# Kernel tuning notes

Measured on AMD Instinct MI355X. Metric: run time of the kernel, lower is better.

The kernel has to match this reference:

```python
import jax, jax.numpy as jnp
import numpy as np
from functools import partial

B, C, COND, L_MEL, HOP, UP = 4, 32, 80, 2048, 8, 8
LAYERS, K, HID, KPK, EMB = 4, 3, 64, 3, 512
L_AUD = L_MEL * UP  # 16384


def conv1d(x, w, b=None, padding=0, dilation=1):
    # x: (B, Cin, L), w: (Cout, Cin, K) -- PyTorch Conv1d semantics
    out = jax.lax.conv_general_dilated(
        x, w, window_strides=(1,), padding=[(padding, padding)],
        rhs_dilation=(dilation,), dimension_numbers=('NCH', 'OIH', 'NCH'))
    if b is not None:
        out = out + b[None, :, None]
    return out


def conv_transpose1d(x, w, stride, pad):
    # PyTorch ConvTranspose1d, weight (Cin, Cout, K), no bias, output_padding=0
    k = w.shape[-1]
    w_eq = jnp.flip(w, -1).transpose(1, 0, 2)  # (Cout, Cin, K)
    lo = k - 1 - pad
    return jax.lax.conv_general_dilated(
        x, w_eq, window_strides=(1,), padding=[(lo, lo)],
        lhs_dilation=(stride,), dimension_numbers=('NCH', 'OIH', 'NCH'))


def lrelu(x, s):
    return jnp.where(x >= 0, x, s * x)


def kernel_predictor(cond, kp_in_w, kp_in_b, kp_res_w1, kp_res_b1,
                     kp_res_w2, kp_res_b2, kp_k_w, kp_k_b, kp_b_w, kp_b_b):
    # FastDiff/UnivNet KernelPredictor: input conv (k=5) + 3 residual blocks + heads
    h = lrelu(conv1d(cond, kp_in_w, kp_in_b, padding=2), 0.1)
    for i in range(3):  # fixed small structural loop
        r = lrelu(conv1d(h, kp_res_w1[i], kp_res_b1[i], padding=1), 0.1)
        r = lrelu(conv1d(r, kp_res_w2[i], kp_res_b2[i], padding=1), 0.1)
        h = h + r
    bsz, _, ln = cond.shape
    k = conv1d(h, kp_k_w, kp_k_b, padding=1)
    b = conv1d(h, kp_b_w, kp_b_b, padding=1)
    kernels = k.reshape(bsz, LAYERS, C, 2 * C, K, ln)
    bias = b.reshape(bsz, LAYERS, 2 * C, ln)
    return kernels, bias


def location_variable_convolution(x, kernel, bias, dilation, hop):
    # x: (B, Cin, L), kernel: (B, Cin, Cout, K, Lf), bias: (B, Cout, Lf)
    bsz, cin, ln = x.shape
    _, _, cout, ks, lf = kernel.shape
    pad = dilation * (ks - 1) // 2
    xp = jnp.pad(x, ((0, 0), (0, 0), (pad, pad)))
    # gather per-frame sliding windows: (Lf, hop, K)
    pos = (jnp.arange(lf) * hop)[:, None, None] \
        + jnp.arange(hop)[None, :, None] \
        + (jnp.arange(ks) * dilation)[None, None, :]
    xw = xp[:, :, pos]  # (B, Cin, Lf, hop, K)
    o = jnp.einsum('bilsk,biokl->bols', xw, kernel)  # (B, Cout, Lf, hop)
    o = o + bias[:, :, :, None]
    return o.reshape(bsz, cout, lf * hop)


def forward(x, audio_down, c, noise_embedding, fc_t_w, fc_t_b, up_w, conv_w,
            kp_in_w, kp_in_b, kp_res_w1, kp_res_b1, kp_res_w2, kp_res_b2,
            kp_k_w, kp_k_b, kp_b_w, kp_b_b):
    noise = (noise_embedding @ fc_t_w.T + fc_t_b)[:, :, None]  # (B, 80, 1)
    condition = c + noise
    kernels, bias = kernel_predictor(condition, kp_in_w, kp_in_b, kp_res_w1,
                                     kp_res_b1, kp_res_w2, kp_res_b2,
                                     kp_k_w, kp_k_b, kp_b_w, kp_b_b)
    h = lrelu(x, 0.2)
    h = conv_transpose1d(h, up_w, UP, UP // 2)  # (B, 32, 16384)
    for i in range(LAYERS):
        h = h + audio_down
        y = lrelu(h, 0.2)
        y = conv1d(y, conv_w[i], padding=3 ** i, dilation=3 ** i)
        y = lrelu(y, 0.2)
        y = location_variable_convolution(y, kernels[:, i], bias[:, i], 1, HOP)
        h = h + jax.nn.sigmoid(y[:, :C, :]) * jnp.tanh(y[:, C:, :])
    return h


def setup_inputs() -> dict:
    key = jax.random.key(0)
    ks = jax.random.split(key, 20)
    s = 0.02
    kch = LAYERS * C * (2 * C) * K  # 24576
    bch = LAYERS * 2 * C            # 256
    return {
        'x': jax.random.normal(ks[0], (B, C, L_MEL), jnp.float32),
        'audio_down': jax.random.normal(ks[1], (B, C, L_AUD), jnp.float32),
        'c': jax.random.normal(ks[2], (B, COND, L_MEL), jnp.float32),
        'noise_embedding': jax.random.normal(ks[3], (B, EMB), jnp.float32),
        'fc_t_w': jax.random.normal(ks[4], (COND, EMB), jnp.float32) * s,
        'fc_t_b': jnp.zeros((COND,), jnp.float32),
        'up_w': jax.random.normal(ks[5], (C, C, UP * 2), jnp.float32) * s,
        'conv_w': jax.random.normal(ks[6], (LAYERS, C, C, K), jnp.float32) * s,
        'kp_in_w': jax.random.normal(ks[7], (HID, COND, 5), jnp.float32) * s,
        'kp_in_b': jnp.zeros((HID,), jnp.float32),
        'kp_res_w1': jax.random.normal(ks[8], (3, HID, HID, KPK), jnp.float32) * s,
        'kp_res_b1': jnp.zeros((3, HID), jnp.float32),
        'kp_res_w2': jax.random.normal(ks[9], (3, HID, HID, KPK), jnp.float32) * s,
        'kp_res_b2': jnp.zeros((3, HID), jnp.float32),
        'kp_k_w': jax.random.normal(ks[10], (kch, HID, KPK), jnp.float32) * s,
        'kp_k_b': jnp.zeros((kch,), jnp.float32),
        'kp_b_w': jax.random.normal(ks[11], (bch, HID, KPK), jnp.float32) * s,
        'kp_b_b': jnp.zeros((bch,), jnp.float32),
    }


def reference(x, audio_down, c, noise_embedding, fc_t_w, fc_t_b, up_w, conv_w,
              kp_in_w, kp_in_b, kp_res_w1, kp_res_b1, kp_res_w2, kp_res_b2,
              kp_k_w, kp_k_b, kp_b_w, kp_b_b):
    return forward(x, audio_down, c, noise_embedding, fc_t_w, fc_t_b, up_w,
                   conv_w, kp_in_w, kp_in_b, kp_res_w1, kp_res_b1, kp_res_w2,
                   kp_res_b2, kp_k_w, kp_k_b, kp_b_w, kp_b_b)
```

## Files before the change

kernel.cpp:

```cpp
#include <hip/hip_runtime.h>
#include <math.h>

#define B_      4
#define C_      32
#define COND_   80
#define LMEL_   2048
#define HOP_    8
#define UP_     8
#define LAYERS_ 4
#define K_      3
#define HID_    64
#define KPK_    3
#define EMB_    512
#define LAUD_   (LMEL_*UP_)
#define KCH_    (LAYERS_*C_*2*C_*K_)
#define BCH_    (LAYERS_*2*C_)

typedef short v8s __attribute__((ext_vector_type(8)));
typedef float v4f __attribute__((ext_vector_type(4)));

__device__ __forceinline__ float lrelu_(float v, float s) { return v >= 0.f ? v : s * v; }

__device__ __forceinline__ unsigned short f2bf(float f) {
  unsigned int x = __float_as_uint(f);
  unsigned int r = (x + 0x7FFFu + ((x >> 16) & 1u)) >> 16;
  return (unsigned short)r;
}

__global__ void k_noise_cond(const float* __restrict__ ne, const float* __restrict__ fw,
                             const float* __restrict__ fb, const float* __restrict__ c,
                             float* __restrict__ cond) {
  int b = blockIdx.x / COND_;
  int cc = blockIdx.x % COND_;
  __shared__ float red[256];
  float p = 0.f;
  for (int j = threadIdx.x; j < EMB_; j += 256)
    p += ne[b*EMB_ + j] * fw[cc*EMB_ + j];
  red[threadIdx.x] = p;
  __syncthreads();
  for (int s = 128; s > 0; s >>= 1) {
    if (threadIdx.x < s) red[threadIdx.x] += red[threadIdx.x + s];
    __syncthreads();
  }
  float noise = red[0] + fb[cc];
  const float* cp = c + (b*COND_ + cc)*LMEL_;
  float* op = cond + (b*COND_ + cc)*LMEL_;
  for (int l = threadIdx.x; l < LMEL_; l += 256) op[l] = cp[l] + noise;
}

__global__ __launch_bounds__(256) void k_kp_in(const float* __restrict__ cond, const float* __restrict__ w,
                                               const float* __restrict__ bias, float* __restrict__ out) {
  const int T = 32;
  int b  = blockIdx.x / (LMEL_/T);
  int lb = (blockIdx.x % (LMEL_/T)) * T;
  __shared__ float sc[COND_][T + 4];
  for (int idx = threadIdx.x; idx < COND_*(T+4); idx += 256) {
    int cc = idx / (T+4), j = idx % (T+4);
    int l = lb + j - 2;
    sc[cc][j] = (l >= 0 && l < LMEL_) ? cond[(b*COND_ + cc)*LMEL_ + l] : 0.f;
  }
  __syncthreads();
  int ch = threadIdx.x & 63;
  int lq = threadIdx.x >> 6;
  float acc[8];
#pragma unroll
  for (int ii = 0; ii < 8; ii++) acc[ii] = bias[ch];
  const float* wr = w + ch*COND_*5;
  for (int cc = 0; cc < COND_; cc++) {
    float r[12];
#pragma unroll
    for (int j = 0; j < 12; j++) r[j] = sc[cc][lq*8 + j];
#pragma unroll
    for (int k = 0; k < 5; k++) {
      float wv = wr[cc*5 + k];
#pragma unroll
      for (int ii = 0; ii < 8; ii++) acc[ii] = fmaf(wv, r[ii + k], acc[ii]);
    }
  }
  float* op = out + (b*HID_ + ch)*LMEL_ + lb + lq*8;
#pragma unroll
  for (int ii = 0; ii < 8; ii++) acc[ii] = lrelu_(acc[ii], 0.1f);
  *reinterpret_cast<float4*>(&op[0]) = make_float4(acc[0], acc[1], acc[2], acc[3]);
  *reinterpret_cast<float4*>(&op[4]) = make_float4(acc[4], acc[5], acc[6], acc[7]);
}

__global__ __launch_bounds__(256) void k_kp_res(const float* __restrict__ in, const float* __restrict__ w,
                                                const float* __restrict__ bias, const float* __restrict__ res,
                                                float* __restrict__ out) {
  const int T = 32;
  int b  = blockIdx.x / (LMEL_/T);
  int lb = (blockIdx.x % (LMEL_/T)) * T;
  __shared__ float si[HID_][T + 4];
  for (int idx = threadIdx.x; idx < HID_*(T+2); idx += 256) {
    int cc = idx / (T+2), j = idx % (T+2);
    int l = lb + j - 1;
    si[cc][j] = (l >= 0 && l < LMEL_) ? in[(b*HID_ + cc)*LMEL_ + l] : 0.f;
  }
  __syncthreads();
  int ch = threadIdx.x & 63;
  int lq = threadIdx.x >> 6;
  float acc[8];
#pragma unroll
  for (int ii = 0; ii < 8; ii++) acc[ii] = bias[ch];
  const float* wr = w + ch*HID_*3;
  for (int cc = 0; cc < HID_; cc++) {
    float r[10];
#pragma unroll
    for (int j = 0; j < 10; j++) r[j] = si[cc][lq*8 + j];
#pragma unroll
    for (int k = 0; k < 3; k++) {
      float wv = wr[cc*3 + k];
#pragma unroll
      for (int ii = 0; ii < 8; ii++) acc[ii] = fmaf(wv, r[ii + k], acc[ii]);
    }
  }
  int lo = lb + lq*8;
  float* op = out + (b*HID_ + ch)*LMEL_ + lo;
  const float* rp = res ? res + (b*HID_ + ch)*LMEL_ + lo : nullptr;
#pragma unroll
  for (int ii = 0; ii < 8; ii++) {
    acc[ii] = lrelu_(acc[ii], 0.1f);
    if (rp) acc[ii] += rp[ii];
  }
  *reinterpret_cast<float4*>(&op[0]) = make_float4(acc[0], acc[1], acc[2], acc[3]);
  *reinterpret_cast<float4*>(&op[4]) = make_float4(acc[4], acc[5], acc[6], acc[7]);
}

__global__ __launch_bounds__(256) void k_kp_bias(const float* __restrict__ in, const float* __restrict__ w,
                                                 const float* __restrict__ bias, float* __restrict__ out) {
  const int T = 16;
  int b  = blockIdx.x / (LMEL_/T);
  int lb = (blockIdx.x % (LMEL_/T)) * T;
  __shared__ float si[HID_][T + 2];
  for (int idx = threadIdx.x; idx < HID_*(T+2); idx += 256) {
    int cc = idx / (T+2), j = idx % (T+2);
    int l = lb + j - 1;
    si[cc][j] = (l >= 0 && l < LMEL_) ? in[(b*HID_ + cc)*LMEL_ + l] : 0.f;
  }
  __syncthreads();
  int ch = threadIdx.x;
  float acc[T];
  float bv = bias[ch];
#pragma unroll
  for (int ii = 0; ii < T; ii++) acc[ii] = bv;
  const float* wr = w + ch*HID_*3;
  for (int cc = 0; cc < HID_; cc++) {
    float w0 = wr[cc*3], w1 = wr[cc*3+1], w2 = wr[cc*3+2];
#pragma unroll
    for (int ii = 0; ii < T; ii++)
      acc[ii] = fmaf(w0, si[cc][ii], fmaf(w1, si[cc][ii+1], fmaf(w2, si[cc][ii+2], acc[ii])));
  }
  float* op = out + (b*BCH_ + ch)*LMEL_ + lb;
#pragma unroll
  for (int q = 0; q < 4; q++)
    *reinterpret_cast<float4*>(&op[q*4]) = make_float4(acc[q*4], acc[q*4+1], acc[q*4+2], acc[q*4+3]);
}

__global__ void k_mkUp(const float* __restrict__ upw, float* __restrict__ wt) {
  int idx = blockIdx.x*256 + threadIdx.x;
  if (idx >= C_*C_*16) return;
  int co = idx & 31, j = (idx >> 5) & 15, ci = idx >> 9;
  wt[idx] = upw[(ci*C_ + co)*16 + j];
}

#define UT 32
__global__ __launch_bounds__(256) void k_upsample(const float* __restrict__ x, const float* __restrict__ wt,
                                                  float* __restrict__ h) {
  int b  = blockIdx.x / 65;
  int s0 = (blockIdx.x % 65) * UT;
  __shared__ float sw[16384];
  __shared__ float sx[C_][33 + 3];
  for (int idx = threadIdx.x*4; idx < 16384; idx += 1024)
    *reinterpret_cast<float4*>(&sw[idx]) = *reinterpret_cast<const float4*>(&wt[idx]);
  for (int idx = threadIdx.x; idx < C_*33; idx += 256) {
    int ci = idx / 33, i = idx % 33;
    int s = s0 - 1 + i;
    float v = (s >= 0 && s < LMEL_) ? x[(b*C_ + ci)*LMEL_ + s] : 0.f;
    sx[ci][i] = lrelu_(v, 0.2f);
  }
  __syncthreads();
  int co = threadIdx.x & 31, sq = threadIdx.x >> 5;
  float acc[4][8];
#pragma unroll
  for (int k = 0; k < 4; k++)
#pragma unroll
    for (int r = 0; r < 8; r++) acc[k][r] = 0.f;
  for (int ci = 0; ci < C_; ci++) {
    float xv[5];
#pragma unroll
    for (int m = 0; m < 5; m++) xv[m] = sx[ci][sq*4 + m];
    const float* wl = &sw[ci*512 + co];
#pragma unroll
    for (int r = 0; r < 8; r++) {
      float wa = wl[r*32];
      float wb = wl[(r+8)*32];
#pragma unroll
      for (int k = 0; k < 4; k++)
        acc[k][r] = fmaf(wa, xv[k+1], fmaf(wb, xv[k], acc[k][r]));
    }
  }
  float* op = h + ((size_t)b*C_ + co)*LAUD_;
#pragma unroll
  for (int k = 0; k < 4; k++) {
    int s1 = s0 + sq*4 + k;
    int lo = 8*s1 - 4;
    if (lo >= 0 && lo + 4 <= LAUD_)
      *reinterpret_cast<float4*>(&op[lo]) = make_float4(acc[k][0], acc[k][1], acc[k][2], acc[k][3]);
    if (lo >= -4 && lo + 8 <= LAUD_)
      *reinterpret_cast<float4*>(&op[lo+4]) = make_float4(acc[k][4], acc[k][5], acc[k][6], acc[k][7]);
  }
}

__global__ void k_mkA(const float* __restrict__ kw, unsigned short* __restrict__ waf) {
  int idx = blockIdx.x*256 + threadIdx.x;
  if (idx >= KCH_*HID_*KPK_) return;
  int i    = idx & 7;
  int lane = (idx >> 3) & 63;
  int ks   = (idx >> 9) % 6;
  int tile = (idx / 3072) & 3;
  int rk   = idx / 12288;
  int layer = rk / 96, rem = rk % 96, ci = rem / 3, kk = rem % 3;
  int cout = tile*16 + (lane & 15);
  int j    = ks*32 + ((lane >> 4) << 3) + i;
  int row  = ((layer*32 + ci)*64 + cout)*3 + kk;
  waf[idx] = f2bf(kw[row*192 + j]);
}

__global__ void k_mkKbT(const float* __restrict__ kb, float* __restrict__ kbt) {
  int idx = blockIdx.x*256 + threadIdx.x;
  if (idx >= KCH_) return;
  int cr = idx & 15, tile = (idx >> 4) & 3, rk = idx >> 6;
  int layer = rk / 96, rem = rk % 96, ci = rem / 3, kk = rem % 3;
  int cout = tile*16 + cr;
  kbt[idx] = kb[((layer*32 + ci)*64 + cout)*3 + kk];
}

template<int DIL>
__global__ __launch_bounds__(256) void k_dilconv(const float* __restrict__ h, const float* __restrict__ ad,
                                                 const float* __restrict__ w, float* __restrict__ y2) {
  const int T = 128;
  int b  = blockIdx.x / (LAUD_/T);
  int tb = (blockIdx.x % (LAUD_/T)) * T;
  const int W = T + 2*DIL;
  __shared__ float ss[C_][T + 2*27 + 4];
  for (int idx = threadIdx.x; idx < C_*W; idx += 256) {
    int ci = idx / W, j = idx % W;
    int t = tb - DIL + j;
    float v = 0.f;
    if (t >= 0 && t < LAUD_) {
      int g = (b*C_ + ci)*LAUD_ + t;
      v = h[g] + ad[g];
    }
    ss[ci][j] = lrelu_(v, 0.2f);
  }
  __syncthreads();
  int co = threadIdx.x & 31, tq = threadIdx.x >> 5;
  float acc[16];
#pragma unroll
  for (int ii = 0; ii < 16; ii++) acc[ii] = 0.f;
  const float* wr = w + co*C_*3;
  for (int ci = 0; ci < C_; ci++) {
    float w0 = wr[ci*3], w1 = wr[ci*3+1], w2 = wr[ci*3+2];
#pragma unroll
    for (int ii = 0; ii < 16; ii++) {
      int tl = tq*16 + ii;
      acc[ii] = fmaf(w0, ss[ci][tl], fmaf(w1, ss[ci][tl + DIL], fmaf(w2, ss[ci][tl + 2*DIL], acc[ii])));
    }
  }
  float* op = y2 + (b*C_ + co)*LAUD_ + tb + tq*16;
#pragma unroll
  for (int ii = 0; ii < 16; ii++) acc[ii] = lrelu_(acc[ii], 0.2f);
#pragma unroll
  for (int q = 0; q < 4; q++)
    *reinterpret_cast<float4*>(&op[q*4]) = make_float4(acc[q*4], acc[q*4+1], acc[q*4+2], acc[q*4+3]);
}

#define FR2 32

#define EPILOGUE(G, OO)                                                          \
  {                                                                              \
    if (G) __syncthreads();                                                      \
    if (wave >= 4) {                                                             \
      _Pragma("unroll") for (int r = 0; r < 4; r++)                              \
        _Pragma("unroll") for (int s = 0; s < 8; s++)                            \
          red[tile][lane][r*8 + s] = OO[r][s];                                   \
    }                                                                            \
    __syncthreads();                                                             \
    if (wave < 4) {                                                              \
      _Pragma("unroll") for (int r = 0; r < 4; r++) {                            \
        int cout = tile*16 + ((lane >> 4) << 2) + r;                             \
        float bv = biasb[((size_t)b*BCH_ + layer*2*C_ + cout)*LMEL_ + l0 + G*16 + f]; \
        _Pragma("unroll") for (int s = 0; s < 8; s++)                            \
          OO[r][s] += red[tile][lane][r*8 + s] + bv;                             \
      }                                                                          \
      if (wave >= 2) {                                                           \
        _Pragma("unroll") for (int r = 0; r < 4; r++)                            \
          _Pragma("unroll") for (int s = 0; s < 8; s++)                          \
            red[tile][lane][r*8 + s] = OO[r][s];                                 \
      }                                                                          \
    }                                                                            \
    __syncthreads();                                                             \
    if (wave < 2) {                                                              \
      _Pragma("unroll") for (int r = 0; r < 4; r++) {                            \
        int cout = tile*16 + ((lane >> 4) << 2) + r;                             \
        size_t base = ((size_t)b*C_ + cout)*LAUD_ + (size_t)(l0 + G*16 + f)*HOP_;\
        float4 h0 = *reinterpret_cast<const float4*>(&h[base]);                  \
        float4 h1 = *reinterpret_cast<const float4*>(&h[base + 4]);              \
        float4 a0 = *reinterpret_cast<const float4*>(&ad[base]);                 \
        float4 a1 = *reinterpret_cast<const float4*>(&ad[base + 4]);             \
        float outv[8];                                                           \
        _Pragma("unroll") for (int s = 0; s < 8; s++) {                          \
          float v  = OO[r][s];                                                   \
          float tv = red[tile + 2][lane][r*8 + s];                               \
          float sig = 1.f / (1.f + __expf(-v));                                  \
          float th  = 1.f - 2.f / (1.f + __expf(2.f*tv));                        \
          float hv = (s < 4) ? ((const float*)&h0)[s] : ((const float*)&h1)[s-4];\
          float av = (s < 4) ? ((const float*)&a0)[s] : ((const float*)&a1)[s-4];\
          outv[s] = hv + av + sig * th;                                          \
        }                                                                        \
        *reinterpret_cast<float4*>(&h[base])     = make_float4(outv[0], outv[1], outv[2], outv[3]); \
        *reinterpret_cast<float4*>(&h[base + 4]) = make_float4(outv[4], outv[5], outv[6], outv[7]); \
      }                                                                          \
    }                                                                            \
  }

__global__ __launch_bounds__(512, 2) void k_lvc_mfma(
    const float* __restrict__ hkp, const unsigned short* __restrict__ waf,
    const float* __restrict__ kbt, const float* __restrict__ biasb,
    const float* __restrict__ y2, const float* __restrict__ ad,
    float* __restrict__ h, int layer) {
  int b  = blockIdx.x >> 6;
  int l0 = (blockIdx.x & 63) * FR2;

  __shared__ __align__(16) float sy[C_][FR2*HOP_ + 4];
  __shared__ __align__(16) float shh[HID_][36];
  __shared__ __align__(16) unsigned short FB[2*6*64*8];
  __shared__ float red[4][64][33];

  int tid = threadIdx.x;
  for (int idx = tid; idx < C_*(FR2*HOP_+2); idx += 512) {
    int ci = idx / (FR2*HOP_+2), j = idx % (FR2*HOP_+2);
    int t = l0*HOP_ - 1 + j;
    sy[ci][j] = (t >= 0 && t < LAUD_) ? y2[(b*C_ + ci)*LAUD_ + t] : 0.f;
  }
  for (int idx = tid; idx < HID_*34; idx += 512) {
    int hh = idx / 34, j = idx % 34;
    int l = l0 - 1 + j;
    shh[hh][j] = (l >= 0 && l < LMEL_) ? hkp[(b*HID_ + hh)*LMEL_ + l] : 0.f;
  }
  __syncthreads();
  for (int idx = tid; idx < 6144; idx += 512) {
    int i = idx & 7, lane2 = (idx >> 3) & 63, gk = idx >> 9;
    int ks = gk % 6, g = gk / 6;
    int k = ks*32 + ((lane2 >> 4) << 3) + i;
    int col = lane2 & 15;
    int hh = k / 3, q = k - hh*3;
    FB[idx] = f2bf(shh[hh][g*16 + col + q]);
  }
  __syncthreads();

  int wave = tid >> 6, lane = tid & 63;
  int tile = wave & 3, cihalf = wave >> 2;
  int f = lane & 15;

  v8s bfrA[6], bfrB[6];
#pragma unroll
  for (int ks = 0; ks < 6; ks++) {
    bfrA[ks] = *reinterpret_cast<const v8s*>(&FB[(ks*64 + lane)*8]);
    bfrB[ks] = *reinterpret_cast<const v8s*>(&FB[((6 + ks)*64 + lane)*8]);
  }

  float o0[4][8], o1[4][8];
#pragma unroll
  for (int r = 0; r < 4; r++)
#pragma unroll
    for (int s = 0; s < 8; s++) { o0[r][s] = 0.f; o1[r][s] = 0.f; }

  const int rk0 = layer*96 + cihalf*48;
  const unsigned short* wbase = waf + ((size_t)rk0*4 + tile)*3072 + lane*8;
  const float* kbbase = kbt + (rk0*4 + tile)*16 + ((lane >> 4) << 2);

  for (int ci16 = 0; ci16 < 16; ci16++) {
    int ci = cihalf*16 + ci16;
    float syr0[12], syr1[12];
    {
      float4 s0 = *reinterpret_cast<const float4*>(&sy[ci][f*8]);
      float4 s1 = *reinterpret_cast<const float4*>(&sy[ci][f*8 + 4]);
      float4 s2 = *reinterpret_cast<const float4*>(&sy[ci][f*8 + 8]);
      syr0[0]=s0.x; syr0[1]=s0.y; syr0[2]=s0.z; syr0[3]=s0.w;
      syr0[4]=s1.x; syr0[5]=s1.y; syr0[6]=s1.z; syr0[7]=s1.w;
      syr0[8]=s2.x; syr0[9]=s2.y; syr0[10]=s2.z; syr0[11]=s2.w;
      float4 t0 = *reinterpret_cast<const float4*>(&sy[ci][(16 + f)*8]);
      float4 t1 = *reinterpret_cast<const float4*>(&sy[ci][(16 + f)*8 + 4]);
      float4 t2 = *reinterpret_cast<const float4*>(&sy[ci][(16 + f)*8 + 8]);
      syr1[0]=t0.x; syr1[1]=t0.y; syr1[2]=t0.z; syr1[3]=t0.w;
      syr1[4]=t1.x; syr1[5]=t1.y; syr1[6]=t1.z; syr1[7]=t1.w;
      syr1[8]=t2.x; syr1[9]=t2.y; syr1[10]=t2.z; syr1[11]=t2.w;
    }
#pragma unroll
    for (int kk = 0; kk < 3; kk++) {
      const unsigned short* wp = wbase + (size_t)(ci16*3 + kk)*12288;
      v4f acc0 = {0.f, 0.f, 0.f, 0.f};
      v4f acc1 = {0.f, 0.f, 0.f, 0.f};
#pragma unroll
      for (int ks = 0; ks < 6; ks++) {
        v8s a = *reinterpret_cast<const v8s*>(wp + ks*512);
        acc0 = __builtin_amdgcn_mfma_f32_16x16x32_bf16(a, bfrA[ks], acc0, 0, 0, 0);
        acc1 = __builtin_amdgcn_mfma_f32_16x16x32_bf16(a, bfrB[ks], acc1, 0, 0, 0);
      }
      float4 kb4 = *reinterpret_cast<const float4*>(kbbase + (ci16*3 + kk)*64);
#pragma unroll
      for (int r = 0; r < 4; r++) {
        float k0 = acc0[r] + ((const float*)&kb4)[r];
        float k1 = acc1[r] + ((const float*)&kb4)[r];
#pragma unroll
        for (int s = 0; s < 8; s++) {
          o0[r][s] = fmaf(k0, syr0[kk + s], o0[r][s]);
          o1[r][s] = fmaf(k1, syr1[kk + s], o1[r][s]);
        }
      }
    }
  }

  EPILOGUE(0, o0)
  EPILOGUE(1, o1)
}

extern "C" void kernel_launch(void* const* d_in, const int* in_sizes, int n_in,
                              void* d_out, int out_size, void* d_ws, size_t ws_size,
                              hipStream_t stream) {
  const float* x     = (const float*)d_in[0];
  const float* ad    = (const float*)d_in[1];
  const float* c     = (const float*)d_in[2];
  const float* ne    = (const float*)d_in[3];
  const float* fw    = (const float*)d_in[4];
  const float* fb    = (const float*)d_in[5];
  const float* upw   = (const float*)d_in[6];
  const float* convw = (const float*)d_in[7];
  const float* kinw  = (const float*)d_in[8];
  const float* kinb  = (const float*)d_in[9];
  const float* krw1  = (const float*)d_in[10];
  const float* krb1  = (const float*)d_in[11];
  const float* krw2  = (const float*)d_in[12];
  const float* krb2  = (const float*)d_in[13];
  const float* kkw   = (const float*)d_in[14];
  const float* kkb   = (const float*)d_in[15];
  const float* kbw   = (const float*)d_in[16];
  const float* kbb   = (const float*)d_in[17];
  float* h = (float*)d_out;

  float* ws = (float*)d_ws;
  float* cond  = ws; ws += B_*COND_*LMEL_;
  float* hkpa  = ws; ws += B_*HID_*LMEL_;
  float* hkpb  = ws; ws += B_*HID_*LMEL_;
  float* biasb = ws; ws += B_*BCH_*LMEL_;
  float* y2    = ws; ws += B_*C_*LAUD_;
  float* kbt   = ws; ws += KCH_;
  float* wtup  = ws; ws += C_*C_*16;
  unsigned short* waf = (unsigned short*)ws; ws += (KCH_*HID_*KPK_)/2;

  k_mkA<<<(KCH_*HID_*KPK_ + 255)/256, 256, 0, stream>>>(kkw, waf);
  k_mkKbT<<<(KCH_ + 255)/256, 256, 0, stream>>>(kkb, kbt);
  k_mkUp<<<(C_*C_*16 + 255)/256, 256, 0, stream>>>(upw, wtup);
  k_noise_cond<<<B_*COND_, 256, 0, stream>>>(ne, fw, fb, c, cond);
  k_kp_in<<<B_*(LMEL_/32), 256, 0, stream>>>(cond, kinw, kinb, hkpa);
  for (int i = 0; i < 3; i++) {
    k_kp_res<<<B_*(LMEL_/32), 256, 0, stream>>>(hkpa, krw1 + i*HID_*HID_*3, krb1 + i*HID_, nullptr, hkpb);
    k_kp_res<<<B_*(LMEL_/32), 256, 0, stream>>>(hkpb, krw2 + i*HID_*HID_*3, krb2 + i*HID_, hkpa, hkpa);
  }
  k_kp_bias<<<B_*(LMEL_/16), 256, 0, stream>>>(hkpa, kbw, kbb, biasb);
  k_upsample<<<B_*65, 256, 0, stream>>>(x, wtup, h);

  for (int i = 0; i < LAYERS_; i++) {
    const float* wci = convw + i*C_*C_*3;
    switch (i) {
      case 0: k_dilconv<1 ><<<B_*(LAUD_/128), 256, 0, stream>>>(h, ad, wci, y2); break;
      case 1: k_dilconv<3 ><<<B_*(LAUD_/128), 256, 0, stream>>>(h, ad, wci, y2); break;
      case 2: k_dilconv<9 ><<<B_*(LAUD_/128), 256, 0, stream>>>(h, ad, wci, y2); break;
      case 3: k_dilconv<27><<<B_*(LAUD_/128), 256, 0, stream>>>(h, ad, wci, y2); break;
    }
    k_lvc_mfma<<<B_*(LMEL_/FR2), 512, 0, stream>>>(hkpa, waf, kbt, biasb, y2, ad, h, i);
  }
}
```

Measured before the change: 483.1 us.

## Fuse residual conv pairs, transpose conv weights, and widen LVC kernel to 1024 threads

Each kernel-predictor residual block now runs as one kernel that computes both convs with a halo and keeps the intermediate in shared memory, replacing two launches and a global round trip. Conv weights are pre-transposed so adjacent threads load contiguous weights. The LVC MFMA kernel goes from 512 to 1024 threads, splitting input channels over four wave groups instead of two, with a serialized multi-step shared-memory reduction and a padded shared layout to reduce bank conflicts. The extra reduction barriers and the larger block may lower occupancy, and the lower launch-bounds register budget could cause spills.

```diff
diff --git a/kernel.cpp b/kernel.cpp
--- a/kernel.cpp
+++ b/kernel.cpp
@@ -27,6 +27,15 @@
   return (unsigned short)r;
 }
 
+__global__ void k_mkWTs(const float* __restrict__ src, float* __restrict__ dst,
+                        int S, int OC, int ICK) {
+  int idx = blockIdx.x*256 + threadIdx.x;
+  if (idx >= S*OC*ICK) return;
+  int s = idx / (OC*ICK), rem = idx % (OC*ICK);
+  int oc = rem / ICK, ick = rem % ICK;
+  dst[s*OC*ICK + ick*OC + oc] = src[idx];
+}
+
 __global__ void k_noise_cond(const float* __restrict__ ne, const float* __restrict__ fw,
                              const float* __restrict__ fb, const float* __restrict__ c,
                              float* __restrict__ cond) {
@@ -48,7 +57,7 @@
   for (int l = threadIdx.x; l < LMEL_; l += 256) op[l] = cp[l] + noise;
 }
 
-__global__ __launch_bounds__(256) void k_kp_in(const float* __restrict__ cond, const float* __restrict__ w,
+__global__ __launch_bounds__(256) void k_kp_in(const float* __restrict__ cond, const float* __restrict__ wT,
                                                const float* __restrict__ bias, float* __restrict__ out) {
   const int T = 32;
   int b  = blockIdx.x / (LMEL_/T);
@@ -65,14 +74,13 @@
   float acc[8];
 #pragma unroll
   for (int ii = 0; ii < 8; ii++) acc[ii] = bias[ch];
-  const float* wr = w + ch*COND_*5;
   for (int cc = 0; cc < COND_; cc++) {
     float r[12];
 #pragma unroll
     for (int j = 0; j < 12; j++) r[j] = sc[cc][lq*8 + j];
 #pragma unroll
     for (int k = 0; k < 5; k++) {
-      float wv = wr[cc*5 + k];
+      float wv = wT[(cc*5 + k)*64 + ch];
 #pragma unroll
       for (int ii = 0; ii < 8; ii++) acc[ii] = fmaf(wv, r[ii + k], acc[ii]);
     }
@@ -84,49 +92,73 @@
   *reinterpret_cast<float4*>(&op[4]) = make_float4(acc[4], acc[5], acc[6], acc[7]);
 }
 
-__global__ __launch_bounds__(256) void k_kp_res(const float* __restrict__ in, const float* __restrict__ w,
-                                                const float* __restrict__ bias, const float* __restrict__ res,
-                                                float* __restrict__ out) {
+__global__ __launch_bounds__(256) void k_kp_res2(const float* __restrict__ in,
+                                                 const float* __restrict__ w1T, const float* __restrict__ b1,
+                                                 const float* __restrict__ w2T, const float* __restrict__ b2,
+                                                 float* __restrict__ out) {
   const int T = 32;
   int b  = blockIdx.x / (LMEL_/T);
   int lb = (blockIdx.x % (LMEL_/T)) * T;
-  __shared__ float si[HID_][T + 4];
-  for (int idx = threadIdx.x; idx < HID_*(T+2); idx += 256) {
-    int cc = idx / (T+2), j = idx % (T+2);
-    int l = lb + j - 1;
+  __shared__ float si[HID_][38];
+  __shared__ float sr[HID_][38];
+  for (int idx = threadIdx.x; idx < HID_*36; idx += 256) {
+    int cc = idx / 36, j = idx % 36;
+    int l = lb - 2 + j;
     si[cc][j] = (l >= 0 && l < LMEL_) ? in[(b*HID_ + cc)*LMEL_ + l] : 0.f;
   }
   __syncthreads();
   int ch = threadIdx.x & 63;
   int lq = threadIdx.x >> 6;
-  float acc[8];
-#pragma unroll
-  for (int ii = 0; ii < 8; ii++) acc[ii] = bias[ch];
-  const float* wr = w + ch*HID_*3;
-  for (int cc = 0; cc < HID_; cc++) {
-    float r[10];
-#pragma unroll
-    for (int j = 0; j < 10; j++) r[j] = si[cc][lq*8 + j];
-#pragma unroll
-    for (int k = 0; k < 3; k++) {
-      float wv = wr[cc*3 + k];
-#pragma unroll
-      for (int ii = 0; ii < 8; ii++) acc[ii] = fmaf(wv, r[ii + k], acc[ii]);
-    }
-  }
-  int lo = lb + lq*8;
-  float* op = out + (b*HID_ + ch)*LMEL_ + lo;
-  const float* rp = res ? res + (b*HID_ + ch)*LMEL_ + lo : nullptr;
-#pragma unroll
-  for (int ii = 0; ii < 8; ii++) {
-    acc[ii] = lrelu_(acc[ii], 0.1f);
-    if (rp) acc[ii] += rp[ii];
-  }
-  *reinterpret_cast<float4*>(&op[0]) = make_float4(acc[0], acc[1], acc[2], acc[3]);
-  *reinterpret_cast<float4*>(&op[4]) = make_float4(acc[4], acc[5], acc[6], acc[7]);
-}
-
-__global__ __launch_bounds__(256) void k_kp_bias(const float* __restrict__ in, const float* __restrict__ w,
+  {
+    float b1v = b1[ch];
+    float a1[9];
+#pragma unroll
+    for (int jj = 0; jj < 9; jj++) a1[jj] = b1v;
+    for (int cc = 0; cc < HID_; cc++) {
+      float r[11];
+#pragma unroll
+      for (int j = 0; j < 11; j++) r[j] = si[cc][lq*9 + j];
+#pragma unroll
+      for (int k = 0; k < 3; k++) {
+        float wv = w1T[(cc*3 + k)*64 + ch];
+#pragma unroll
+        for (int jj = 0; jj < 9; jj++) a1[jj] = fmaf(wv, r[jj + k], a1[jj]);
+      }
+    }
+#pragma unroll
+    for (int jj = 0; jj < 9; jj++) {
+      int m = lq*9 + jj;
+      if (m < 34) sr[ch][m] = lrelu_(a1[jj], 0.1f);
+    }
+  }
+  __syncthreads();
+  {
+    float b2v = b2[ch];
+    float a2[8];
+#pragma unroll
+    for (int jj = 0; jj < 8; jj++) a2[jj] = b2v;
+    for (int cc = 0; cc < HID_; cc++) {
+      float r[10];
+#pragma unroll
+      for (int j = 0; j < 10; j++) r[j] = sr[cc][lq*8 + j];
+#pragma unroll
+      for (int k = 0; k < 3; k++) {
+        float wv = w2T[(cc*3 + k)*64 + ch];
+#pragma unroll
+        for (int jj = 0; jj < 8; jj++) a2[jj] = fmaf(wv, r[jj + k], a2[jj]);
+      }
+    }
+    float* op = out + (b*HID_ + ch)*LMEL_ + lb + lq*8;
+    float v[8];
+#pragma unroll
+    for (int jj = 0; jj < 8; jj++)
+      v[jj] = si[ch][lq*8 + jj + 2] + lrelu_(a2[jj], 0.1f);
+    *reinterpret_cast<float4*>(&op[0]) = make_float4(v[0], v[1], v[2], v[3]);
+    *reinterpret_cast<float4*>(&op[4]) = make_float4(v[4], v[5], v[6], v[7]);
+  }
+}
+
+__global__ __launch_bounds__(256) void k_kp_bias(const float* __restrict__ in, const float* __restrict__ wT,
                                                  const float* __restrict__ bias, float* __restrict__ out) {
   const int T = 16;
   int b  = blockIdx.x / (LMEL_/T);
@@ -143,9 +175,10 @@
   float bv = bias[ch];
 #pragma unroll
   for (int ii = 0; ii < T; ii++) acc[ii] = bv;
-  const float* wr = w + ch*HID_*3;
   for (int cc = 0; cc < HID_; cc++) {
-    float w0 = wr[cc*3], w1 = wr[cc*3+1], w2 = wr[cc*3+2];
+    float w0 = wT[(cc*3 + 0)*256 + ch];
+    float w1 = wT[(cc*3 + 1)*256 + ch];
+    float w2 = wT[(cc*3 + 2)*256 + ch];
 #pragma unroll
     for (int ii = 0; ii < T; ii++)
       acc[ii] = fmaf(w0, si[cc][ii], fmaf(w1, si[cc][ii+1], fmaf(w2, si[cc][ii+2], acc[ii])));
@@ -237,7 +270,7 @@
 
 template<int DIL>
 __global__ __launch_bounds__(256) void k_dilconv(const float* __restrict__ h, const float* __restrict__ ad,
-                                                 const float* __restrict__ w, float* __restrict__ y2) {
+                                                 const float* __restrict__ wT, float* __restrict__ y2) {
   const int T = 128;
   int b  = blockIdx.x / (LAUD_/T);
   int tb = (blockIdx.x % (LAUD_/T)) * T;
@@ -258,9 +291,10 @@
   float acc[16];
 #pragma unroll
   for (int ii = 0; ii < 16; ii++) acc[ii] = 0.f;
-  const float* wr = w + co*C_*3;
   for (int ci = 0; ci < C_; ci++) {
-    float w0 = wr[ci*3], w1 = wr[ci*3+1], w2 = wr[ci*3+2];
+    float w0 = wT[(ci*3 + 0)*32 + co];
+    float w1 = wT[(ci*3 + 1)*32 + co];
+    float w2 = wT[(ci*3 + 2)*32 + co];
 #pragma unroll
     for (int ii = 0; ii < 16; ii++) {
       int tl = tq*16 + ii;
@@ -276,27 +310,41 @@
 }
 
 #define FR2 32
+#define SYC(c) ((c) + (((c) >> 5) << 2))
+#define RED(t, l, rs) pool[(((t)*64 + (l))*33) + (rs)]
 
 #define EPILOGUE(G, OO)                                                          \
   {                                                                              \
-    if (G) __syncthreads();                                                      \
-    if (wave >= 4) {                                                             \
+    __syncthreads();                                                             \
+    if (wq == 3) {                                                               \
       _Pragma("unroll") for (int r = 0; r < 4; r++)                              \
         _Pragma("unroll") for (int s = 0; s < 8; s++)                            \
-          red[tile][lane][r*8 + s] = OO[r][s];                                   \
+          RED(tile, lane, r*8 + s) = OO[r][s];                                   \
     }                                                                            \
     __syncthreads();                                                             \
-    if (wave < 4) {                                                              \
+    if (wq == 2) {                                                               \
+      _Pragma("unroll") for (int r = 0; r < 4; r++)                              \
+        _Pragma("unroll") for (int s = 0; s < 8; s++)                            \
+          RED(tile, lane, r*8 + s) += OO[r][s];                                  \
+    }                                                                            \
+    __syncthreads();                                                             \
+    if (wq == 1) {                                                               \
+      _Pragma("unroll") for (int r = 0; r < 4; r++)                              \
+        _Pragma("unroll") for (int s = 0; s < 8; s++)                            \
+          RED(tile, lane, r*8 + s) += OO[r][s];                                  \
+    }                                                                            \
+    __syncthreads();                                                             \
+    if (wq == 0) {                                                               \
       _Pragma("unroll") for (int r = 0; r < 4; r++) {                            \
         int cout = tile*16 + ((lane >> 4) << 2) + r;                             \
         float bv = biasb[((size_t)b*BCH_ + layer*2*C_ + cout)*LMEL_ + l0 + G*16 + f]; \
         _Pragma("unroll") for (int s = 0; s < 8; s++)                            \
-          OO[r][s] += red[tile][lane][r*8 + s] + bv;                             \
+          OO[r][s] += RED(tile, lane, r*8 + s) + bv;                             \
       }                                                                          \
-      if (wave >= 2) {                                                           \
+      if (tile >= 2) {                                                           \
         _Pragma("unroll") for (int r = 0; r < 4; r++)                            \
           _Pragma("unroll") for (int s = 0; s < 8; s++)                          \
-            red[tile][lane][r*8 + s] = OO[r][s];                                 \
+            RED(tile, lane, r*8 + s) = OO[r][s];                                 \
       }                                                                          \
     }                                                                            \
     __syncthreads();                                                             \
@@ -311,7 +359,7 @@
         float outv[8];                                                           \
         _Pragma("unroll") for (int s = 0; s < 8; s++) {                          \
           float v  = OO[r][s];                                                   \
-          float tv = red[tile + 2][lane][r*8 + s];                               \
+          float tv = RED(tile + 2, lane, r*8 + s);                               \
           float sig = 1.f / (1.f + __expf(-v));                                  \
           float th  = 1.f - 2.f / (1.f + __expf(2.f*tv));                        \
           float hv = (s < 4) ? ((const float*)&h0)[s] : ((const float*)&h1)[s-4];\
@@ -324,7 +372,7 @@
     }                                                                            \
   }
 
-__global__ __launch_bounds__(512, 2) void k_lvc_mfma(
+__global__ __launch_bounds__(1024) void k_lvc_mfma(
     const float* __restrict__ hkp, const unsigned short* __restrict__ waf,
     const float* __restrict__ kbt, const float* __restrict__ biasb,
     const float* __restrict__ y2, const float* __restrict__ ad,
@@ -332,24 +380,23 @@
   int b  = blockIdx.x >> 6;
   int l0 = (blockIdx.x & 63) * FR2;
 
-  __shared__ __align__(16) float sy[C_][FR2*HOP_ + 4];
+  __shared__ __align__(16) float pool[32*292];
   __shared__ __align__(16) float shh[HID_][36];
   __shared__ __align__(16) unsigned short FB[2*6*64*8];
-  __shared__ float red[4][64][33];
 
   int tid = threadIdx.x;
-  for (int idx = tid; idx < C_*(FR2*HOP_+2); idx += 512) {
+  for (int idx = tid; idx < C_*(FR2*HOP_+2); idx += 1024) {
     int ci = idx / (FR2*HOP_+2), j = idx % (FR2*HOP_+2);
     int t = l0*HOP_ - 1 + j;
-    sy[ci][j] = (t >= 0 && t < LAUD_) ? y2[(b*C_ + ci)*LAUD_ + t] : 0.f;
-  }
-  for (int idx = tid; idx < HID_*34; idx += 512) {
+    pool[ci*292 + SYC(j)] = (t >= 0 && t < LAUD_) ? y2[(b*C_ + ci)*LAUD_ + t] : 0.f;
+  }
+  for (int idx = tid; idx < HID_*34; idx += 1024) {
     int hh = idx / 34, j = idx % 34;
     int l = l0 - 1 + j;
     shh[hh][j] = (l >= 0 && l < LMEL_) ? hkp[(b*HID_ + hh)*LMEL_ + l] : 0.f;
   }
   __syncthreads();
-  for (int idx = tid; idx < 6144; idx += 512) {
+  for (int idx = tid; idx < 6144; idx += 1024) {
     int i = idx & 7, lane2 = (idx >> 3) & 63, gk = idx >> 9;
     int ks = gk % 6, g = gk / 6;
     int k = ks*32 + ((lane2 >> 4) << 3) + i;
@@ -360,7 +407,7 @@
   __syncthreads();
 
   int wave = tid >> 6, lane = tid & 63;
-  int tile = wave & 3, cihalf = wave >> 2;
+  int tile = wave & 3, wq = wave >> 2;
   int f = lane & 15;
 
   v8s bfrA[6], bfrB[6];
@@ -376,30 +423,32 @@
 #pragma unroll
     for (int s = 0; s < 8; s++) { o0[r][s] = 0.f; o1[r][s] = 0.f; }
 
-  const int rk0 = layer*96 + cihalf*48;
+  const int rk0 = layer*96 + wq*24;
   const unsigned short* wbase = waf + ((size_t)rk0*4 + tile)*3072 + lane*8;
   const float* kbbase = kbt + (rk0*4 + tile)*16 + ((lane >> 4) << 2);
 
-  for (int ci16 = 0; ci16 < 16; ci16++) {
-    int ci = cihalf*16 + ci16;
+  for (int ciq = 0; ciq < 8; ciq++) {
+    int ci = wq*8 + ciq;
+    const float* syrow = &pool[ci*292];
     float syr0[12], syr1[12];
     {
-      float4 s0 = *reinterpret_cast<const float4*>(&sy[ci][f*8]);
-      float4 s1 = *reinterpret_cast<const float4*>(&sy[ci][f*8 + 4]);
-      float4 s2 = *reinterpret_cast<const float4*>(&sy[ci][f*8 + 8]);
+      int c0 = f*8, c1 = 128 + f*8;
+      float4 s0 = *reinterpret_cast<const float4*>(&syrow[SYC(c0)]);
+      float4 s1 = *reinterpret_cast<const float4*>(&syrow[SYC(c0+4)]);
+      float4 s2 = *reinterpret_cast<const float4*>(&syrow[SYC(c0+8)]);
       syr0[0]=s0.x; syr0[1]=s0.y; syr0[2]=s0.z; syr0[3]=s0.w;
       syr0[4]=s1.x; syr0[5]=s1.y; syr0[6]=s1.z; syr0[7]=s1.w;
       syr0[8]=s2.x; syr0[9]=s2.y; syr0[10]=s2.z; syr0[11]=s2.w;
-      float4 t0 = *reinterpret_cast<const float4*>(&sy[ci][(16 + f)*8]);
-      float4 t1 = *reinterpret_cast<const float4*>(&sy[ci][(16 + f)*8 + 4]);
-      float4 t2 = *reinterpret_cast<const float4*>(&sy[ci][(16 + f)*8 + 8]);
+      float4 t0 = *reinterpret_cast<const float4*>(&syrow[SYC(c1)]);
+      float4 t1 = *reinterpret_cast<const float4*>(&syrow[SYC(c1+4)]);
+      float4 t2 = *reinterpret_cast<const float4*>(&syrow[SYC(c1+8)]);
       syr1[0]=t0.x; syr1[1]=t0.y; syr1[2]=t0.z; syr1[3]=t0.w;
       syr1[4]=t1.x; syr1[5]=t1.y; syr1[6]=t1.z; syr1[7]=t1.w;
       syr1[8]=t2.x; syr1[9]=t2.y; syr1[10]=t2.z; syr1[11]=t2.w;
     }
 #pragma unroll
     for (int kk = 0; kk < 3; kk++) {
-      const unsigned short* wp = wbase + (size_t)(ci16*3 + kk)*12288;
+      const unsigned short* wp = wbase + (size_t)(ciq*3 + kk)*12288;
       v4f acc0 = {0.f, 0.f, 0.f, 0.f};
       v4f acc1 = {0.f, 0.f, 0.f, 0.f};
 #pragma unroll
@@ -408,7 +457,7 @@
         acc0 = __builtin_amdgcn_mfma_f32_16x16x32_bf16(a, bfrA[ks], acc0, 0, 0, 0);
         acc1 = __builtin_amdgcn_mfma_f32_16x16x32_bf16(a, bfrB[ks], acc1, 0, 0, 0);
       }
-      float4 kb4 = *reinterpret_cast<const float4*>(kbbase + (ci16*3 + kk)*64);
+      float4 kb4 = *reinterpret_cast<const float4*>(kbbase + (ciq*3 + kk)*64);
 #pragma unroll
       for (int r = 0; r < 4; r++) {
         float k0 = acc0[r] + ((const float*)&kb4)[r];
@@ -450,35 +499,48 @@
   float* h = (float*)d_out;
 
   float* ws = (float*)d_ws;
-  float* cond  = ws; ws += B_*COND_*LMEL_;
-  float* hkpa  = ws; ws += B_*HID_*LMEL_;
-  float* hkpb  = ws; ws += B_*HID_*LMEL_;
-  float* biasb = ws; ws += B_*BCH_*LMEL_;
-  float* y2    = ws; ws += B_*C_*LAUD_;
-  float* kbt   = ws; ws += KCH_;
-  float* wtup  = ws; ws += C_*C_*16;
+  float* cond   = ws; ws += B_*COND_*LMEL_;
+  float* hkpa   = ws; ws += B_*HID_*LMEL_;
+  float* hkpb   = ws; ws += B_*HID_*LMEL_;
+  float* biasb  = ws; ws += B_*BCH_*LMEL_;
+  float* y2     = ws; ws += B_*C_*LAUD_;
+  float* kbt    = ws; ws += KCH_;
+  float* wtup   = ws; ws += C_*C_*16;
+  float* kinwT  = ws; ws += HID_*COND_*5;
+  float* krw1T  = ws; ws += 3*HID_*HID_*3;
+  float* krw2T  = ws; ws += 3*HID_*HID_*3;
+  float* kbwT   = ws; ws += BCH_*HID_*3;
+  float* convwT = ws; ws += LAYERS_*C_*C_*3;
   unsigned short* waf = (unsigned short*)ws; ws += (KCH_*HID_*KPK_)/2;
 
   k_mkA<<<(KCH_*HID_*KPK_ + 255)/256, 256, 0, stream>>>(kkw, waf);
   k_mkKbT<<<(KCH_ + 255)/256, 256, 0, stream>>>(kkb, kbt);
   k_mkUp<<<(C_*C_*16 + 255)/256, 256, 0, stream>>>(upw, wtup);
+  k_mkWTs<<<(HID_*COND_*5 + 255)/256, 256, 0, stream>>>(kinw, kinwT, 1, HID_, COND_*5);
+  k_mkWTs<<<(3*HID_*HID_*3 + 255)/256, 256, 0, stream>>>(krw1, krw1T, 3, HID_, HID_*3);
+  k_mkWTs<<<(3*HID_*HID_*3 + 255)/256, 256, 0, stream>>>(krw2, krw2T, 3, HID_, HID_*3);
+  k_mkWTs<<<(BCH_*HID_*3 + 255)/256, 256, 0, stream>>>(kbw, kbwT, 1, BCH_, HID_*3);
+  k_mkWTs<<<(LAYERS_*C_*C_*3 + 255)/256, 256, 0, stream>>>(convw, convwT, LAYERS_, C_, C_*3);
+
   k_noise_cond<<<B_*COND_, 256, 0, stream>>>(ne, fw, fb, c, cond);
-  k_kp_in<<<B_*(LMEL_/32), 256, 0, stream>>>(cond, kinw, kinb, hkpa);
-  for (int i = 0; i < 3; i++) {
-    k_kp_res<<<B_*(LMEL_/32), 256, 0, stream>>>(hkpa, krw1 + i*HID_*HID_*3, krb1 + i*HID_, nullptr, hkpb);
-    k_kp_res<<<B_*(LMEL_/32), 256, 0, stream>>>(hkpb, krw2 + i*HID_*HID_*3, krb2 + i*HID_, hkpa, hkpa);
-  }
-  k_kp_bias<<<B_*(LMEL_/16), 256, 0, stream>>>(hkpa, kbw, kbb, biasb);
+  k_kp_in<<<B_*(LMEL_/32), 256, 0, stream>>>(cond, kinwT, kinb, hkpa);
+  k_kp_res2<<<B_*(LMEL_/32), 256, 0, stream>>>(hkpa, krw1T + 0*HID_*HID_*3, krb1 + 0*HID_,
+                                               krw2T + 0*HID_*HID_*3, krb2 + 0*HID_, hkpb);
+  k_kp_res2<<<B_*(LMEL_/32), 256, 0, stream>>>(hkpb, krw1T + 1*HID_*HID_*3, krb1 + 1*HID_,
+                                               krw2T + 1*HID_*HID_*3, krb2 + 1*HID_, hkpa);
+  k_kp_res2<<<B_*(LMEL_/32), 256, 0, stream>>>(hkpa, krw1T + 2*HID_*HID_*3, krb1 + 2*HID_,
+                                               krw2T + 2*HID_*HID_*3, krb2 + 2*HID_, hkpb);
+  k_kp_bias<<<B_*(LMEL_/16), 256, 0, stream>>>(hkpb, kbwT, kbb, biasb);
   k_upsample<<<B_*65, 256, 0, stream>>>(x, wtup, h);
 
   for (int i = 0; i < LAYERS_; i++) {
-    const float* wci = convw + i*C_*C_*3;
+    const float* wci = convwT + i*C_*C_*3;
     switch (i) {
       case 0: k_dilconv<1 ><<<B_*(LAUD_/128), 256, 0, stream>>>(h, ad, wci, y2); break;
       case 1: k_dilconv<3 ><<<B_*(LAUD_/128), 256, 0, stream>>>(h, ad, wci, y2); break;
       case 2: k_dilconv<9 ><<<B_*(LAUD_/128), 256, 0, stream>>>(h, ad, wci, y2); break;
       case 3: k_dilconv<27><<<B_*(LAUD_/128), 256, 0, stream>>>(h, ad, wci, y2); break;
     }
-    k_lvc_mfma<<<B_*(LMEL_/FR2), 512, 0, stream>>>(hkpa, waf, kbt, biasb, y2, ad, h, i);
-  }
-}
+    k_lvc_mfma<<<B_*(LMEL_/FR2), 1024, 0, stream>>>(hkpb, waf, kbt, biasb, y2, ad, h, i);
+  }
+}
```

Result: slower. 1.085 ms (+124.5%).
